# Performance work log

Hardware: AMD Instinct MI355X
Metric: run time of the kernel (lower is better)

Reference implementation:

```python
import jax, jax.numpy as jnp
import numpy as np

ALPHA = 0.2  # LeakyReLU negative slope
N, IN_DIM, OUT_DIM = 8192, 512, 64


def setup_inputs() -> dict:
    key = jax.random.key(0)
    k1, k2, k3, k4 = jax.random.split(key, 4)
    X = jax.random.normal(k1, (N, IN_DIM), dtype=jnp.float32)
    Adj = jax.random.randint(k2, (N, N), 0, 2, dtype=jnp.int32)
    # xavier_uniform with gain=1.414
    def xavier(k, shape, gain=1.414):
        fan_in, fan_out = shape[0], shape[1]
        bound = gain * np.sqrt(6.0 / (fan_in + fan_out))
        return jax.random.uniform(k, shape, jnp.float32, -bound, bound)
    W = xavier(k3, (IN_DIM, OUT_DIM))
    a = xavier(k4, (2 * OUT_DIM, 1))
    return {"X": X, "Adj": Adj, "W": W, "a": a}


def reference(X, Adj, W, a):
    # h = X @ W : [N, D]
    h = X @ W
    D = h.shape[1]
    # Decompose pairwise score: concat([h_i, h_j]) @ a == h_i @ a1 + h_j @ a2
    s1 = h @ a[:D, 0]   # [N] -- contribution of row (destination) node i
    s2 = h @ a[D:, 0]   # [N] -- contribution of column (source) node j
    e = jnp.exp(jax.nn.leaky_relu(s1[:, None] + s2[None, :], negative_slope=ALPHA))  # [N, N]
    e = jnp.where(Adj == 0, jnp.float32(0.0), e)
    attention = e / jnp.sum(e, axis=1, keepdims=True)
    # dropout is a no-op in eval mode (training=False)
    return attention @ h
```

## Files before the change

kernel.cpp:

```cpp
#include <hip/hip_runtime.h>
#include <math.h>


#define NN 8192
#define KIN 512
#define DD 64
#define ALPHA 0.2f

using floatx4 = __attribute__((ext_vector_type(4))) float;
using bf16x8  = __attribute__((ext_vector_type(8))) __bf16;

__global__ __launch_bounds__(256) void k_gemm_h(const float* __restrict__ X,
                                                const float* __restrict__ W,
                                                float* __restrict__ h) {
    __shared__ __align__(16) float XT[32 * 36];
    __shared__ __align__(16) float WL[32 * 64];
    const int t = threadIdx.x;
    const int i0 = blockIdx.x * 32;
    const int rb = t >> 5;
    const int db = t & 31;
    float acc[4][2] = {};

    for (int k0 = 0; k0 < KIN; k0 += 32) {
        {
            const int row = t >> 3, kq = t & 7;
            const float4 x4 = *(const float4*)(X + (size_t)(i0 + row) * KIN + k0 + kq * 4);
            XT[(kq * 4 + 0) * 36 + row] = x4.x;
            XT[(kq * 4 + 1) * 36 + row] = x4.y;
            XT[(kq * 4 + 2) * 36 + row] = x4.z;
            XT[(kq * 4 + 3) * 36 + row] = x4.w;
#pragma unroll
            for (int p = 0; p < 2; ++p) {
                const int q = p * 256 + t;
                const int kk = q >> 4, dq = q & 15;
                *(float4*)(WL + kk * 64 + dq * 4) =
                    *(const float4*)(W + (size_t)(k0 + kk) * DD + dq * 4);
            }
        }
        __syncthreads();
#pragma unroll
        for (int k = 0; k < 32; ++k) {
            const float4 xa = *(const float4*)(XT + k * 36 + rb * 4);
            const float2 wb = *(const float2*)(WL + k * 64 + db * 2);
            const float xv[4] = {xa.x, xa.y, xa.z, xa.w};
#pragma unroll
            for (int i = 0; i < 4; ++i) {
                acc[i][0] += xv[i] * wb.x;
                acc[i][1] += xv[i] * wb.y;
            }
        }
        __syncthreads();
    }
#pragma unroll
    for (int i = 0; i < 4; ++i) {
        float2 o = {acc[i][0], acc[i][1]};
        *(float2*)(h + (size_t)(i0 + rb * 4 + i) * DD + db * 2) = o;
    }
}

__global__ __launch_bounds__(256) void k_s12(const float* __restrict__ h,
                                             const float* __restrict__ a,
                                             float* __restrict__ s1,
                                             float* __restrict__ s2) {
    const int lane = threadIdx.x & 63;
    const int w = threadIdx.x >> 6;
    const int r = blockIdx.x * 4 + w;
    const float v = h[(size_t)r * DD + lane];
    float p1 = v * a[lane];
    float p2 = v * a[64 + lane];
#pragma unroll
    for (int off = 32; off; off >>= 1) {
        p1 += __shfl_xor(p1, off, 64);
        p2 += __shfl_xor(p2, off, 64);
    }
    if (lane == 0) {
        s1[r] = p1;
        s2[r] = p2;
    }
}

__global__ __launch_bounds__(256) void k_hfrag(const float* __restrict__ h,
                                               __bf16* __restrict__ hFrag) {
    const int f = blockIdx.x * 256 + threadIdx.x;
    const int lane = f & 63, dt = (f >> 6) & 3, jblk = f >> 8;
    const int n = lane & 15, q = lane >> 4;
    bf16x8 v;
#pragma unroll
    for (int jj = 0; jj < 8; ++jj)
        v[jj] = (__bf16)h[(size_t)(jblk * 32 + q * 8 + jj) * DD + dt * 16 + n];
    *(bf16x8*)(hFrag + (size_t)f * 8) = v;
}

__global__ __launch_bounds__(256) void k_attn2(const bf16x8* __restrict__ hFrag,
                                               const int* __restrict__ Adj,
                                               const float* __restrict__ s1,
                                               const float* __restrict__ s2,
                                               float* __restrict__ numP,
                                               float* __restrict__ denP) {
    const int t = threadIdx.x;
    const int wv = t >> 6;
    const int lane = t & 63;
    const int n = lane & 15, q = lane >> 4;
    const int it = blockIdx.x >> 3, jc = blockIdx.x & 7;
    const int i0 = it * 64;
    const int row = i0 + wv * 16 + n;
    const float s1v = s1[row];
    const int jbase = jc * 1024;

    floatx4 acc[4] = {};
    float den = 0.f;

    const int* adjRow = Adj + (size_t)row * NN;

    for (int ks = 0; ks < 32; ++ks) {
        const int j0 = jbase + ks * 32;
        const int jq = j0 + q * 8;
        const int4 a0 = *(const int4*)(adjRow + jq);
        const int4 a1 = *(const int4*)(adjRow + jq + 4);
        const float4 z0 = *(const float4*)(s2 + jq);
        const float4 z1 = *(const float4*)(s2 + jq + 4);
        const int adjv[8] = {a0.x, a0.y, a0.z, a0.w, a1.x, a1.y, a1.z, a1.w};
        const float s2v[8] = {z0.x, z0.y, z0.z, z0.w, z1.x, z1.y, z1.z, z1.w};
        bf16x8 af;
#pragma unroll
        for (int u = 0; u < 8; ++u) {
            const float s = s1v + s2v[u];
            const float l = fmaxf(s, ALPHA * s);
            float e = __expf(l);
            e = adjv[u] ? e : 0.f;
            den += e;
            af[u] = (__bf16)e;
        }
        const bf16x8* hf = hFrag + ((size_t)(j0 >> 5) * 4) * 64 + lane;
#pragma unroll
        for (int dt = 0; dt < 4; ++dt) {
            const bf16x8 bf = hf[dt * 64];
            acc[dt] = __builtin_amdgcn_mfma_f32_16x16x32_bf16(af, bf, acc[dt], 0, 0, 0);
        }
    }

    const size_t base = (size_t)blockIdx.x * 4096;
#pragma unroll
    for (int dt = 0; dt < 4; ++dt)
#pragma unroll
        for (int r = 0; r < 4; ++r)
            numP[base + (size_t)(wv * 16 + q * 4 + r) * 64 + dt * 16 + n] = acc[dt][r];

    den += __shfl_xor(den, 16, 64);
    den += __shfl_xor(den, 32, 64);
    if (q == 0) denP[(size_t)blockIdx.x * 64 + wv * 16 + n] = den;
}

__global__ __launch_bounds__(256) void k_final(const float* __restrict__ numP,
                                               const float* __restrict__ denP,
                                               float* __restrict__ out) {
    const int idx = blockIdx.x * 256 + threadIdx.x;
    const int i = idx >> 6, d = idx & 63;
    const int it = i >> 6, r = i & 63;
    float num = 0.f, den = 0.f;
#pragma unroll
    for (int c = 0; c < 8; ++c) {
        const size_t bx = (size_t)(it * 8 + c);
        num += numP[bx * 4096 + (size_t)r * 64 + d];
        den += denP[bx * 64 + r];
    }
    out[idx] = num / den;
}

extern "C" void kernel_launch(void* const* d_in, const int* in_sizes, int n_in,
                              void* d_out, int out_size, void* d_ws, size_t ws_size,
                              hipStream_t stream) {
    const float* X = (const float*)d_in[0];
    const int* Adj = (const int*)d_in[1];
    const float* W = (const float*)d_in[2];
    const float* a = (const float*)d_in[3];
    float* out = (float*)d_out;

    float* ws = (float*)d_ws;
    float* h = ws;
    float* s1 = h + 524288;
    float* s2 = s1 + 8192;
    __bf16* hFrag = (__bf16*)(s2 + 8192);
    float* numP = s2 + 8192 + 262144;
    float* denP = numP + 1024 * 4096;

    k_gemm_h<<<256, 256, 0, stream>>>(X, W, h);
    k_s12<<<2048, 256, 0, stream>>>(h, a, s1, s2);
    k_hfrag<<<256, 256, 0, stream>>>(h, hFrag);
    k_attn2<<<1024, 256, 0, stream>>>((const bf16x8*)hFrag, Adj, s1, s2, numP, denP);
    k_final<<<2048, 256, 0, stream>>>(numP, denP, out);
}
```

Measured before the change: 432.3 us.

## Coalesce adjacency loads via LDS-staged attention tiles and MFMA row-sum

Reworks the attention kernel so each wavefront reads contiguous 1KB spans of an adjacency row instead of scattered 32-byte chunks from 16 rows. Exponentiated scores are written to shared memory and reloaded in MFMA fragment layout. The row-sum denominator is computed with an extra MFMA against a ones vector instead of scalar accumulation. This adds LDS traffic and rounds the denominator through bf16.

```diff
diff --git a/kernel.cpp b/kernel.cpp
--- a/kernel.cpp
+++ b/kernel.cpp
@@ -9,6 +9,7 @@
 
 using floatx4 = __attribute__((ext_vector_type(4))) float;
 using bf16x8  = __attribute__((ext_vector_type(8))) __bf16;
+using bf16x4  = __attribute__((ext_vector_type(4))) __bf16;
 
 __global__ __launch_bounds__(256) void k_gemm_h(const float* __restrict__ X,
                                                 const float* __restrict__ W,
@@ -91,51 +92,68 @@
     *(bf16x8*)(hFrag + (size_t)f * 8) = v;
 }
 
-__global__ __launch_bounds__(256) void k_attn2(const bf16x8* __restrict__ hFrag,
-                                               const int* __restrict__ Adj,
-                                               const float* __restrict__ s1,
-                                               const float* __restrict__ s2,
-                                               float* __restrict__ numP,
-                                               float* __restrict__ denP) {
+__global__ __launch_bounds__(256, 4) void k_attn3(const bf16x8* __restrict__ hFrag,
+                                                  const int* __restrict__ Adj,
+                                                  const float* __restrict__ s1,
+                                                  const float* __restrict__ s2,
+                                                  float* __restrict__ numP,
+                                                  float* __restrict__ denP) {
+    __shared__ __align__(16) __bf16 ET[4][16][264];
     const int t = threadIdx.x;
     const int wv = t >> 6;
     const int lane = t & 63;
     const int n = lane & 15, q = lane >> 4;
     const int it = blockIdx.x >> 3, jc = blockIdx.x & 7;
     const int i0 = it * 64;
-    const int row = i0 + wv * 16 + n;
-    const float s1v = s1[row];
-    const int jbase = jc * 1024;
-
-    floatx4 acc[4] = {};
-    float den = 0.f;
-
-    const int* adjRow = Adj + (size_t)row * NN;
-
-    for (int ks = 0; ks < 32; ++ks) {
-        const int j0 = jbase + ks * 32;
-        const int jq = j0 + q * 8;
-        const int4 a0 = *(const int4*)(adjRow + jq);
-        const int4 a1 = *(const int4*)(adjRow + jq + 4);
-        const float4 z0 = *(const float4*)(s2 + jq);
-        const float4 z1 = *(const float4*)(s2 + jq + 4);
-        const int adjv[8] = {a0.x, a0.y, a0.z, a0.w, a1.x, a1.y, a1.z, a1.w};
-        const float s2v[8] = {z0.x, z0.y, z0.z, z0.w, z1.x, z1.y, z1.z, z1.w};
-        bf16x8 af;
-#pragma unroll
-        for (int u = 0; u < 8; ++u) {
-            const float s = s1v + s2v[u];
-            const float l = fmaxf(s, ALPHA * s);
-            float e = __expf(l);
-            e = adjv[u] ? e : 0.f;
-            den += e;
-            af[u] = (__bf16)e;
-        }
-        const bf16x8* hf = hFrag + ((size_t)(j0 >> 5) * 4) * 64 + lane;
-#pragma unroll
-        for (int dt = 0; dt < 4; ++dt) {
-            const bf16x8 bf = hf[dt * 64];
-            acc[dt] = __builtin_amdgcn_mfma_f32_16x16x32_bf16(af, bf, acc[dt], 0, 0, 0);
+
+    float s1v[16];
+#pragma unroll
+    for (int rr = 0; rr < 16; ++rr) s1v[rr] = s1[i0 + wv * 16 + rr];
+
+    bf16x8 ones;
+#pragma unroll
+    for (int u = 0; u < 8; ++u) ones[u] = (__bf16)1.0f;
+
+    floatx4 acc[5] = {};
+
+    const int* adjBase = Adj + (size_t)(i0 + wv * 16) * NN + jc * 1024 + lane * 4;
+
+    for (int w = 0; w < 4; ++w) {
+        const int j0 = jc * 1024 + w * 256;
+        const float4 z = *(const float4*)(s2 + j0 + lane * 4);
+#pragma unroll
+        for (int pass = 0; pass < 4; ++pass) {
+            int4 av[4];
+#pragma unroll
+            for (int r4 = 0; r4 < 4; ++r4)
+                av[r4] = *(const int4*)(adjBase + (size_t)(pass * 4 + r4) * NN + w * 256);
+#pragma unroll
+            for (int r4 = 0; r4 < 4; ++r4) {
+                const int rr = pass * 4 + r4;
+                const float s1r = s1v[rr];
+                const int am[4] = {av[r4].x, av[r4].y, av[r4].z, av[r4].w};
+                const float zz[4] = {z.x, z.y, z.z, z.w};
+                bf16x4 ev;
+#pragma unroll
+                for (int c = 0; c < 4; ++c) {
+                    const float s = s1r + zz[c];
+                    const float l = fmaxf(s, ALPHA * s);
+                    float e = __expf(l);
+                    e = am[c] ? e : 0.f;
+                    ev[c] = (__bf16)e;
+                }
+                *(bf16x4*)&ET[wv][rr][lane * 4] = ev;
+            }
+        }
+        const int jblk0 = j0 >> 5;
+#pragma unroll
+        for (int ks = 0; ks < 8; ++ks) {
+            const bf16x8 af = *(const bf16x8*)&ET[wv][n][ks * 32 + q * 8];
+            const bf16x8* hf = hFrag + ((size_t)(jblk0 + ks) * 4) * 64 + lane;
+#pragma unroll
+            for (int dt = 0; dt < 4; ++dt)
+                acc[dt] = __builtin_amdgcn_mfma_f32_16x16x32_bf16(af, hf[dt * 64], acc[dt], 0, 0, 0);
+            acc[4] = __builtin_amdgcn_mfma_f32_16x16x32_bf16(af, ones, acc[4], 0, 0, 0);
         }
     }
 
@@ -146,9 +164,11 @@
         for (int r = 0; r < 4; ++r)
             numP[base + (size_t)(wv * 16 + q * 4 + r) * 64 + dt * 16 + n] = acc[dt][r];
 
-    den += __shfl_xor(den, 16, 64);
-    den += __shfl_xor(den, 32, 64);
-    if (q == 0) denP[(size_t)blockIdx.x * 64 + wv * 16 + n] = den;
+    if (n == 0) {
+#pragma unroll
+        for (int r = 0; r < 4; ++r)
+            denP[(size_t)blockIdx.x * 64 + wv * 16 + q * 4 + r] = acc[4][r];
+    }
 }
 
 __global__ __launch_bounds__(256) void k_final(const float* __restrict__ numP,
@@ -187,6 +207,6 @@
     k_gemm_h<<<256, 256, 0, stream>>>(X, W, h);
     k_s12<<<2048, 256, 0, stream>>>(h, a, s1, s2);
     k_hfrag<<<256, 256, 0, stream>>>(h, hFrag);
-    k_attn2<<<1024, 256, 0, stream>>>((const bf16x8*)hFrag, Adj, s1, s2, numP, denP);
+    k_attn3<<<1024, 256, 0, stream>>>((const bf16x8*)hFrag, Adj, s1, s2, numP, denP);
     k_final<<<2048, 256, 0, stream>>>(numP, denP, out);
 }
```

Measured after the change: 419.1 us. 3.1% less time.
